# Performance work log

Measured on AMD Instinct MI355X. Metric: run time of the kernel, lower is better.

Reference implementation:

```python
import math
import jax, jax.numpy as jnp
import numpy as np

R = 15  # static Gaussian truncation radius (covers 3*sigma for resolutions up to ~12)
SIG_PER_FWHM = 1.0 / math.sqrt(8.0 * math.log(2.0))  # sigma = fwhm / sqrt(8 ln 2)


def _blur_resample_axis0(img, sigma, res):
    """Gaussian blur (dct2/symmetric boundary) + down/up resize along axis 0.

    img: [H, W]; sigma, res: scalars. anchor='f' resize convention:
      down (factor=1/res): low coord j samples input at j*res
      up   (factor=res, shape=H): out coord i samples low grid at i/res
    Low-res grid has n_low = max(floor(H/res), 1) valid rows; positions are
    clamped to the valid range (edge boundary).
    """
    H, W = img.shape
    dt = img.dtype
    # --- separable 1D Gaussian blur along axis 0 ---
    off = jnp.arange(-R, R + 1, dtype=dt)
    sig = jnp.maximum(sigma, jnp.asarray(1e-6, dt))
    w = jnp.exp(-0.5 * (off / sig) ** 2)
    w = w / w.sum()
    pad = jnp.pad(img, ((R, R), (0, 0)), mode='symmetric')  # dct2 boundary
    s = w[0] * pad[0:H]
    for k in range(1, 2 * R + 1):
        s = s + w[k] * pad[k:k + H]
    # --- downsample (factor = 1/res, anchor 'f') ---
    Hf = jnp.asarray(H, dt)
    n_low = jnp.maximum(jnp.floor(Hf / res), 1.0).astype(jnp.int32)
    pos = jnp.clip(jnp.arange(H, dtype=dt) * res, 0.0, Hf - 1.0)
    lo = jnp.floor(pos)
    fr = (pos - lo)[:, None]
    lo_i = lo.astype(jnp.int32)
    hi_i = jnp.minimum(lo_i + 1, H - 1)
    low = s[lo_i] * (1.0 - fr) + s[hi_i] * fr  # [H, W], rows >= n_low unused
    # --- upsample back to H (factor = res, anchor 'f') ---
    pos2 = jnp.clip(jnp.arange(H, dtype=dt) / res, 0.0, n_low.astype(dt) - 1.0)
    lo2 = jnp.floor(pos2)
    fr2 = (pos2 - lo2)[:, None]
    lo2_i = jnp.minimum(lo2.astype(jnp.int32), n_low - 1)
    hi2_i = jnp.minimum(lo2_i + 1, n_low - 1)
    return low[lo2_i] * (1.0 - fr2) + low[hi2_i] * fr2


def _process_one(img, res, ax, gp):
    fwhm = res * gp
    sigma = fwhm * SIG_PER_FWHM
    out0 = _blur_resample_axis0(img, sigma, res)          # degrade axis 0 (H)
    out1 = _blur_resample_axis0(img.T, sigma, res).T      # degrade axis 1 (W)
    return jnp.where(ax == 0, out0, out1)


def setup_inputs() -> dict:
    key = jax.random.key(0)
    k_x, k_res, k_ax, k_gap = jax.random.split(key, 4)
    B, C, H, W = 16, 4, 512, 512
    x = jax.random.normal(k_x, (B, C, H, W), dtype=jnp.float32)
    # lognormal with mean 3, sd 3 -> underlying normal params
    m, sdev = 3.0, 3.0
    var_log = math.log(1.0 + (sdev / m) ** 2)
    mu = math.log(m) - 0.5 * var_log
    z = jax.random.normal(k_res, (B, C), dtype=jnp.float32)
    resolution = jnp.clip(jnp.exp(mu + math.sqrt(var_log) * z), 1.0, None)
    axis = jax.random.randint(k_ax, (B, C), 0, 2, dtype=jnp.int32)
    gap = jax.random.uniform(k_gap, (B, C), dtype=jnp.float32)
    return {"x": x, "resolution": resolution, "axis": axis, "gap": gap}


def reference(x, resolution, axis, gap):
    B, C, H, W = x.shape
    flat = x.reshape(B * C, H, W)
    out = jax.vmap(_process_one)(flat, resolution.reshape(-1), axis.reshape(-1), gap.reshape(-1))
    return out.reshape(B, C, H, W)
```

## Files before the change

kernel.cpp:

```cpp
#include <hip/hip_runtime.h>
#include <math.h>


#define RR 15
#define TAPS 31
#define SEG0 8
#define SIG_PER_FWHM 0.42466090014400953f

__global__ __launch_bounds__(256) void lowres2d_kernel(
    const float* __restrict__ x,
    const float* __restrict__ resolution,
    const int*   __restrict__ axis,
    const float* __restrict__ gap,
    float* __restrict__ out)
{
    const int tid = threadIdx.x;
    const int n   = blockIdx.y;
    const int bx  = blockIdx.x;

    const float res = resolution[n];
    const int   ax  = axis[n];
    const float gp  = gap[n];

    if (ax == 0 && bx >= 64) return;

    const float sig = fmaxf(res * gp * SIG_PER_FWHM, 1e-6f);
    int n_low = (int)floorf(512.0f / res);
    if (n_low < 1) n_low = 1;
    if (n_low > 512) n_low = 512;
    const float nlm1f = (float)(n_low - 1);

    int kr = (int)(sig * 5.2565f) + 1;
    if (kr > RR) kr = RR;
    const int k0 = RR - kr, k1 = RR + 1 + kr;
    const int la_lo = kr, la_hi = 510 - kr;

    __shared__ float2 wd[32];
    __shared__ float s_img[4][520];
    __shared__ float s_low[4][516];

    if (tid < 32) {
        const int k = tid;
        float r = 0.0f;
        if (k < TAPS) {
            float d = (float)(k - RR) / sig;
            r = expf(-0.5f * d * d);
        }
        float tot = r;
        tot += __shfl_xor(tot, 1, 32);
        tot += __shfl_xor(tot, 2, 32);
        tot += __shfl_xor(tot, 4, 32);
        tot += __shfl_xor(tot, 8, 32);
        tot += __shfl_xor(tot, 16, 32);
        float rm1 = __shfl_up(r, 1, 32);
        if (k == 0) rm1 = 0.0f;
        const float inv = 1.0f / tot;
        wd[k] = make_float2(r * inv, (rm1 - r) * inv);
    }
    __syncthreads();

    const size_t base = (size_t)n * (512 * 512);
    const float* img = x + base;
    float* o = out + base;

    if (ax == 0) {
        const int lt = tid & 127;
        const int g  = __builtin_amdgcn_readfirstlane(tid >> 7);
        const int i0 = bx * SEG0 + g * 4;
        const float4* img4 = (const float4*)img;
        float4* out4 = (float4*)o;

        auto compute_low = [&](int j) -> float4 {
            float pos = fminf((float)j * res, 511.0f);
            float lof = floorf(pos);
            float fr  = pos - lof;
            int   la  = __builtin_amdgcn_readfirstlane((int)lof);
            float4 acc = make_float4(0.0f, 0.0f, 0.0f, 0.0f);
            if (la >= la_lo && la <= la_hi) {
                #pragma unroll 4
                for (int k = k0; k <= k1; ++k) {
                    int t = la - RR + k;
                    float2 w = wd[k];
                    float cw = fmaf(fr, w.y, w.x);
                    float4 v = img4[(size_t)(t * 128 + lt)];
                    acc.x = fmaf(cw, v.x, acc.x);
                    acc.y = fmaf(cw, v.y, acc.y);
                    acc.z = fmaf(cw, v.z, acc.z);
                    acc.w = fmaf(cw, v.w, acc.w);
                }
            } else {
                for (int k = k0; k <= k1; ++k) {
                    int t = la - RR + k;
                    t = (t < 0)   ? (-1 - t)   : t;
                    t = (t > 511) ? (1023 - t) : t;
                    float2 w = wd[k];
                    float cw = fmaf(fr, w.y, w.x);
                    float4 v = img4[(size_t)(t * 128 + lt)];
                    acc.x = fmaf(cw, v.x, acc.x);
                    acc.y = fmaf(cw, v.y, acc.y);
                    acc.z = fmaf(cw, v.z, acc.z);
                    acc.w = fmaf(cw, v.w, acc.w);
                }
            }
            return acc;
        };

        float p0 = fminf((float)i0 / res, nlm1f);
        int j = (int)floorf(p0);
        if (j > n_low - 1) j = n_low - 1;
        j = __builtin_amdgcn_readfirstlane(j);
        float4 lowA = compute_low(j);
        int jB = (j + 1 < n_low) ? (j + 1) : (n_low - 1);
        float4 lowB = (jB == j) ? lowA : compute_low(jB);

        for (int i = i0; i < i0 + 4; ++i) {
            float pos2 = fminf((float)i / res, nlm1f);
            float l2f  = floorf(pos2);
            float fr2  = pos2 - l2f;
            int lo2 = (int)l2f;
            if (lo2 > n_low - 1) lo2 = n_low - 1;

            if (lo2 == j + 1) {
                j = lo2;
                lowA = lowB;
                jB = (j + 1 < n_low) ? (j + 1) : (n_low - 1);
                lowB = (jB == j) ? lowA : compute_low(jB);
            } else if (lo2 > j + 1) {
                j = lo2;
                lowA = compute_low(j);
                jB = (j + 1 < n_low) ? (j + 1) : (n_low - 1);
                lowB = (jB == j) ? lowA : compute_low(jB);
            }
            float omf2 = 1.0f - fr2;
            float4 ov;
            ov.x = lowA.x * omf2 + lowB.x * fr2;
            ov.y = lowA.y * omf2 + lowB.y * fr2;
            ov.z = lowA.z * omf2 + lowB.z * fr2;
            ov.w = lowA.w * omf2 + lowB.w * fr2;
            out4[(size_t)(i * 128 + lt)] = ov;
        }
    } else {
        const int h0 = bx * 4;

        const float4* img4 = (const float4*)(img + (size_t)h0 * 512);
        #pragma unroll
        for (int p = 0; p < 2; ++p) {
            int m = p * 256 + tid;
            int r = m >> 7, c4 = m & 127;
            ((float4*)&s_img[r][0])[c4] = img4[r * 128 + c4];
        }
        __syncthreads();

        {
            const int r = __builtin_amdgcn_readfirstlane(tid >> 6);
            for (int j = (tid & 63); j < n_low; j += 64) {
                float pos = fminf((float)j * res, 511.0f);
                float lof = floorf(pos);
                float fr  = pos - lof;
                int   la  = (int)lof;
                float acc = 0.0f;
                if (la >= la_lo && la <= la_hi) {
                    #pragma unroll 4
                    for (int k = k0; k <= k1; ++k) {
                        int t = la - RR + k;
                        float2 w = wd[k];
                        float cw = fmaf(fr, w.y, w.x);
                        acc = fmaf(cw, s_img[r][t], acc);
                    }
                } else {
                    for (int k = k0; k <= k1; ++k) {
                        int t = la - RR + k;
                        t = (t < 0)   ? (-1 - t)   : t;
                        t = (t > 511) ? (1023 - t) : t;
                        float2 w = wd[k];
                        float cw = fmaf(fr, w.y, w.x);
                        acc = fmaf(cw, s_img[r][t], acc);
                    }
                }
                s_low[r][j] = acc;
            }
        }
        __syncthreads();

        float4* out4 = (float4*)(o + (size_t)h0 * 512);
        #pragma unroll
        for (int p = 0; p < 2; ++p) {
            int m = p * 256 + tid;
            int r = m >> 7, c4 = m & 127;
            float vals[4];
            #pragma unroll
            for (int q = 0; q < 4; ++q) {
                int i = c4 * 4 + q;
                float pos2 = fminf((float)i / res, nlm1f);
                float l2f  = floorf(pos2);
                float fr2  = pos2 - l2f;
                int lo2 = (int)l2f;
                if (lo2 > n_low - 1) lo2 = n_low - 1;
                int hi2 = (lo2 + 1 < n_low) ? (lo2 + 1) : (n_low - 1);
                vals[q] = s_low[r][lo2] * (1.0f - fr2) + s_low[r][hi2] * fr2;
            }
            float4 ov;
            ov.x = vals[0]; ov.y = vals[1]; ov.z = vals[2]; ov.w = vals[3];
            out4[r * 128 + c4] = ov;
        }
    }
}

extern "C" void kernel_launch(void* const* d_in, const int* in_sizes, int n_in,
                              void* d_out, int out_size, void* d_ws, size_t ws_size,
                              hipStream_t stream) {
    const float* x          = (const float*)d_in[0];
    const float* resolution = (const float*)d_in[1];
    const int*   axis       = (const int*)d_in[2];
    const float* gap        = (const float*)d_in[3];
    float* out = (float*)d_out;

    const int n_img = in_sizes[1];

    dim3 grid(128, n_img);
    lowres2d_kernel<<<grid, 256, 0, stream>>>(x, resolution, axis, gap, out);
}
```

Measured before the change: 129.4 us.

## Share low-res rows across 8 output rows via LDS in axis-0 path

In the axis-0 branch, each block now has all 256 threads cover the full 512-wide row as float2 columns. It computes every low-res row needed for its 8 output rows once and stores them in shared memory, then interpolates from there. Before, two 128-thread groups each handled 4 rows with float4 and could recompute the same low-res rows. The change removes that duplicate blur work but adds a barrier and narrower float2 global loads. The shared buffer is aliased with the existing arrays and holds up to 9 rows, which assumes res >= 1 so the span jhi-jlo stays small.

```diff
diff --git a/kernel.cpp b/kernel.cpp
--- a/kernel.cpp
+++ b/kernel.cpp
@@ -4,7 +4,6 @@
 
 #define RR 15
 #define TAPS 31
-#define SEG0 8
 #define SIG_PER_FWHM 0.42466090014400953f
 
 __global__ __launch_bounds__(256) void lowres2d_kernel(
@@ -36,8 +35,10 @@
     const int la_lo = kr, la_hi = 510 - kr;
 
     __shared__ float2 wd[32];
-    __shared__ float s_img[4][520];
-    __shared__ float s_low[4][516];
+    __shared__ float smem[4608];
+    float (*s_img)[520]  = (float (*)[520])smem;
+    float (*s_low)[516]  = (float (*)[516])(smem + 4 * 520);
+    float (*s_lowB)[512] = (float (*)[512])smem;
 
     if (tid < 32) {
         const int k = tid;
@@ -64,29 +65,33 @@
     float* o = out + base;
 
     if (ax == 0) {
-        const int lt = tid & 127;
-        const int g  = __builtin_amdgcn_readfirstlane(tid >> 7);
-        const int i0 = bx * SEG0 + g * 4;
-        const float4* img4 = (const float4*)img;
-        float4* out4 = (float4*)o;
-
-        auto compute_low = [&](int j) -> float4 {
+        const int i0 = bx * 8;
+        const int c  = tid;
+        const float2* img2 = (const float2*)img;
+        float2* out2 = (float2*)o;
+
+        float pA = fminf((float)i0 / res, nlm1f);
+        int jlo = (int)floorf(pA);
+        float pB = fminf((float)(i0 + 7) / res, nlm1f);
+        int jhi = (int)floorf(pB) + 1;
+        if (jhi > n_low - 1) jhi = n_low - 1;
+        if (jhi < jlo) jhi = jlo;
+
+        for (int j = jlo; j <= jhi; ++j) {
             float pos = fminf((float)j * res, 511.0f);
             float lof = floorf(pos);
             float fr  = pos - lof;
-            int   la  = __builtin_amdgcn_readfirstlane((int)lof);
-            float4 acc = make_float4(0.0f, 0.0f, 0.0f, 0.0f);
+            int   la  = (int)lof;
+            float2 acc = make_float2(0.0f, 0.0f);
             if (la >= la_lo && la <= la_hi) {
                 #pragma unroll 4
                 for (int k = k0; k <= k1; ++k) {
                     int t = la - RR + k;
                     float2 w = wd[k];
                     float cw = fmaf(fr, w.y, w.x);
-                    float4 v = img4[(size_t)(t * 128 + lt)];
+                    float2 v = img2[(size_t)(t * 256 + c)];
                     acc.x = fmaf(cw, v.x, acc.x);
                     acc.y = fmaf(cw, v.y, acc.y);
-                    acc.z = fmaf(cw, v.z, acc.z);
-                    acc.w = fmaf(cw, v.w, acc.w);
                 }
             } else {
                 for (int k = k0; k <= k1; ++k) {
@@ -95,49 +100,29 @@
                     t = (t > 511) ? (1023 - t) : t;
                     float2 w = wd[k];
                     float cw = fmaf(fr, w.y, w.x);
-                    float4 v = img4[(size_t)(t * 128 + lt)];
+                    float2 v = img2[(size_t)(t * 256 + c)];
                     acc.x = fmaf(cw, v.x, acc.x);
                     acc.y = fmaf(cw, v.y, acc.y);
-                    acc.z = fmaf(cw, v.z, acc.z);
-                    acc.w = fmaf(cw, v.w, acc.w);
                 }
             }
-            return acc;
-        };
-
-        float p0 = fminf((float)i0 / res, nlm1f);
-        int j = (int)floorf(p0);
-        if (j > n_low - 1) j = n_low - 1;
-        j = __builtin_amdgcn_readfirstlane(j);
-        float4 lowA = compute_low(j);
-        int jB = (j + 1 < n_low) ? (j + 1) : (n_low - 1);
-        float4 lowB = (jB == j) ? lowA : compute_low(jB);
-
-        for (int i = i0; i < i0 + 4; ++i) {
+            ((float2*)&s_lowB[j - jlo][0])[c] = acc;
+        }
+        __syncthreads();
+
+        #pragma unroll
+        for (int ii = 0; ii < 8; ++ii) {
+            int i = i0 + ii;
             float pos2 = fminf((float)i / res, nlm1f);
             float l2f  = floorf(pos2);
             float fr2  = pos2 - l2f;
             int lo2 = (int)l2f;
-            if (lo2 > n_low - 1) lo2 = n_low - 1;
-
-            if (lo2 == j + 1) {
-                j = lo2;
-                lowA = lowB;
-                jB = (j + 1 < n_low) ? (j + 1) : (n_low - 1);
-                lowB = (jB == j) ? lowA : compute_low(jB);
-            } else if (lo2 > j + 1) {
-                j = lo2;
-                lowA = compute_low(j);
-                jB = (j + 1 < n_low) ? (j + 1) : (n_low - 1);
-                lowB = (jB == j) ? lowA : compute_low(jB);
-            }
+            int hi2 = (lo2 + 1 <= jhi) ? (lo2 + 1) : jhi;
+            float2 A = ((float2*)&s_lowB[lo2 - jlo][0])[c];
+            float2 B = ((float2*)&s_lowB[hi2 - jlo][0])[c];
             float omf2 = 1.0f - fr2;
-            float4 ov;
-            ov.x = lowA.x * omf2 + lowB.x * fr2;
-            ov.y = lowA.y * omf2 + lowB.y * fr2;
-            ov.z = lowA.z * omf2 + lowB.z * fr2;
-            ov.w = lowA.w * omf2 + lowB.w * fr2;
-            out4[(size_t)(i * 128 + lt)] = ov;
+            out2[(size_t)(i * 256 + c)] =
+                make_float2(A.x * omf2 + B.x * fr2,
+                            A.y * omf2 + B.y * fr2);
         }
     } else {
         const int h0 = bx * 4;
```

After: 131.8 us. No clear change (+1.8%).
